# Kernel optimization log

Hardware: AMD Instinct MI355X
Metric: run time of the kernel (lower is better)

Reference implementation:

```python
import jax, jax.numpy as jnp
import numpy as np

DEPTH, LENGTH, WIDTH, NUM_CLASSES = 8, 32, 32, 8
STD_POSITION = 1.0
STD_INTENSITY = 3.0


def setup_inputs() -> dict:
    key = jax.random.key(0)
    k1, k2 = jax.random.split(key)
    patch = jax.random.normal(k1, (DEPTH, LENGTH, WIDTH), dtype=jnp.float32)
    prob = jax.random.uniform(k2, (DEPTH, LENGTH, WIDTH, NUM_CLASSES), dtype=jnp.float32)
    return {"patch": patch, "prob": prob, "k": NUM_CLASSES}


def _dist_weight():
    # Matches torch.meshgrid(arange(depth), arange(length), arange(width)) with 'ij' indexing,
    # then row-major flatten. dist_weight[i,j] = exp(-||pos_i - pos_j||^2 / std_position^2)
    gx, gy, gz = jnp.meshgrid(
        jnp.arange(DEPTH, dtype=jnp.float32),
        jnp.arange(LENGTH, dtype=jnp.float32),
        jnp.arange(WIDTH, dtype=jnp.float32),
        indexing="ij",
    )
    x, y, z = gx.ravel(), gy.ravel(), gz.ravel()  # each [n]
    sq = (
        jnp.square(x[:, None] - x[None, :])
        + jnp.square(y[:, None] - y[None, :])
        + jnp.square(z[:, None] - z[None, :])
    )  # [n, n]
    return jnp.exp(-sq / (STD_POSITION ** 2))


def reference(patch, prob, k):
    n = DEPTH * LENGTH * WIDTH
    f = patch.reshape(-1)  # [n]
    # intensity_weight is .detach()ed in the original -> stop_gradient for faithfulness
    intensity = jax.lax.stop_gradient(
        jnp.exp(-jnp.square((f[:, None] - f[None, :]) / STD_INTENSITY))
    )  # [n, n]
    W = intensity * _dist_weight()  # [n, n]

    P = prob.reshape(n, k)  # row-major flatten matches torch.reshape of prob[:,:,:,t]
    WP = W @ P  # [n, k]
    num = jnp.sum(P * WP, axis=0)            # per-class p^T W p
    den = P.T @ (W @ jnp.ones((n,), W.dtype))  # per-class p^T W 1
    loss = jnp.float32(k) - jnp.sum(num / den)
    return loss.astype(jnp.float32)
```

## Files before the change

kernel.cpp:

```cpp
#include <hip/hip_runtime.h>

#define N       8192
#define NCLS    8
#define ROWS_PB 4
#define GRID    (N / ROWS_PB)

__global__ __launch_bounds__(256) void sncut_rows(const float* __restrict__ f,
                                                  const float* __restrict__ P,
                                                  float* __restrict__ partials)
{
    const int tid  = threadIdx.x;
    const int lane = tid & 63;
    const int wave = tid >> 6;
    const int i    = blockIdx.x * ROWS_PB + wave;

    const int zi = i & 31, yi = (i >> 5) & 31, xi = i >> 10;
    const float fi = f[i];

    float v0 = 0.f, v1 = 0.f, v2 = 0.f, v3 = 0.f;
    float v4 = 0.f, v5 = 0.f, v6 = 0.f, v7 = 0.f;
    float vr = 0.f;

    if (lane < 63) {
        const int oy = lane / 9, oz = lane - oy * 9;

        int y0 = yi - 3; y0 = y0 < 0 ? 0 : (y0 > 25 ? 25 : y0);
        int z0 = zi - 4; z0 = z0 < 0 ? 0 : (z0 > 23 ? 23 : z0);
        int x0 = xi - 3; x0 = x0 < 0 ? 0 : (x0 > 1 ? 1 : x0);

        const int yj = y0 + oy, zj = z0 + oz;
        const int dy = yi - yj, dz = zi - zj;
        const float base = (float)(dy * dy + dz * dz);
        const int jcol = (yj << 5) + zj;

        #pragma unroll
        for (int k = 0; k < 7; ++k) {
            const int xj = x0 + k;
            const int dx = xi - xj;
            const int j  = (xj << 10) + jcol;
            const float df  = fi - f[j];
            const float arg = df * df * (1.0f / 9.0f) + (base + (float)(dx * dx));
            const float w   = __expf(-arg);
            const float4 p0 = *reinterpret_cast<const float4*>(P + (size_t)j * NCLS);
            const float4 p1 = *reinterpret_cast<const float4*>(P + (size_t)j * NCLS + 4);
            v0 += w * p0.x; v1 += w * p0.y; v2 += w * p0.z; v3 += w * p0.w;
            v4 += w * p1.x; v5 += w * p1.y; v6 += w * p1.z; v7 += w * p1.w;
            vr += w;
        }
    }

    float vals[9] = {v0, v1, v2, v3, v4, v5, v6, v7, vr};
    #pragma unroll
    for (int v = 0; v < 9; ++v) {
        float x = vals[v];
        #pragma unroll
        for (int off = 32; off > 0; off >>= 1)
            x += __shfl_down(x, off, 64);
        vals[v] = x;
    }

    __shared__ float sh[ROWS_PB][16];
    if (lane == 0) {
        const float4 p0 = *reinterpret_cast<const float4*>(P + (size_t)i * NCLS);
        const float4 p1 = *reinterpret_cast<const float4*>(P + (size_t)i * NCLS + 4);
        sh[wave][0]  = p0.x * vals[0];
        sh[wave][1]  = p0.y * vals[1];
        sh[wave][2]  = p0.z * vals[2];
        sh[wave][3]  = p0.w * vals[3];
        sh[wave][4]  = p1.x * vals[4];
        sh[wave][5]  = p1.y * vals[5];
        sh[wave][6]  = p1.z * vals[6];
        sh[wave][7]  = p1.w * vals[7];
        sh[wave][8]  = p0.x * vals[8];
        sh[wave][9]  = p0.y * vals[8];
        sh[wave][10] = p0.z * vals[8];
        sh[wave][11] = p0.w * vals[8];
        sh[wave][12] = p1.x * vals[8];
        sh[wave][13] = p1.y * vals[8];
        sh[wave][14] = p1.z * vals[8];
        sh[wave][15] = p1.w * vals[8];
    }
    __syncthreads();
    if (tid < 16) {
        const float s = sh[0][tid] + sh[1][tid] + sh[2][tid] + sh[3][tid];
        partials[(size_t)blockIdx.x * 16 + tid] = s;
    }
}

__global__ __launch_bounds__(1024) void sncut_final(const float* __restrict__ partials,
                                                    float* __restrict__ out)
{
    const int tid = threadIdx.x;
    const int e = tid & 15;
    const int g = tid >> 4;

    float s = 0.f;
    #pragma unroll
    for (int m = 0; m < GRID / 64; ++m)
        s += partials[(size_t)(g + m * 64) * 16 + e];

    __shared__ float acc[64][17];
    acc[g][e] = s;
    __syncthreads();

    __shared__ float sums[16];
    if (tid < 16) {
        float t = 0.f;
        #pragma unroll
        for (int g2 = 0; g2 < 64; ++g2) t += acc[g2][tid];
        sums[tid] = t;
    }
    __syncthreads();
    if (tid == 0) {
        float loss = (float)NCLS;
        #pragma unroll
        for (int t = 0; t < NCLS; ++t) loss -= sums[t] / sums[NCLS + t];
        out[0] = loss;
    }
}

extern "C" void kernel_launch(void* const* d_in, const int* in_sizes, int n_in,
                              void* d_out, int out_size, void* d_ws, size_t ws_size,
                              hipStream_t stream) {
    const float* f = (const float*)d_in[0];
    const float* P = (const float*)d_in[1];

    float* partials = (float*)d_ws;

    sncut_rows<<<GRID, 256, 0, stream>>>(f, P, partials);
    sncut_final<<<1, 1024, 0, stream>>>(partials, (float*)d_out);
}
```

Measured before the change: 67.60 us.

## Stage shared neighborhood tile in LDS for eight rows per block

Each block now handles eight consecutive z-rows and first cooperatively loads the union of their 7x7x16 neighborhood (f and P split into float2 planes) into shared memory. The per-row window loop then reads from LDS instead of issuing scattered global loads. This removes redundant global/L2 traffic across neighboring rows but adds a barrier, a staging phase, and larger blocks with more LDS use per block.

```diff
diff --git a/kernel.cpp b/kernel.cpp
--- a/kernel.cpp
+++ b/kernel.cpp
@@ -2,19 +2,49 @@
 
 #define N       8192
 #define NCLS    8
-#define ROWS_PB 4
+#define ROWS_PB 8
 #define GRID    (N / ROWS_PB)
+#define NCELL   784
 
-__global__ __launch_bounds__(256) void sncut_rows(const float* __restrict__ f,
+__global__ __launch_bounds__(512) void sncut_rows(const float* __restrict__ f,
                                                   const float* __restrict__ P,
                                                   float* __restrict__ partials)
 {
+    __shared__ float2 Pl[4][NCELL];
+    __shared__ float  fl[NCELL];
+    __shared__ float  sh[ROWS_PB][16];
+
     const int tid  = threadIdx.x;
     const int lane = tid & 63;
     const int wave = tid >> 6;
-    const int i    = blockIdx.x * ROWS_PB + wave;
+    const int i0   = blockIdx.x * ROWS_PB;
 
-    const int zi = i & 31, yi = (i >> 5) & 31, xi = i >> 10;
+    const int zi0 = i0 & 31;
+    const int yi  = (i0 >> 5) & 31;
+    const int xi  = i0 >> 10;
+
+    int Y0 = yi - 3;  Y0 = Y0 < 0 ? 0 : (Y0 > 25 ? 25 : Y0);
+    int X0 = xi - 3;  X0 = X0 < 0 ? 0 : (X0 > 1 ? 1 : X0);
+    int Z0 = zi0 - 4; Z0 = Z0 < 0 ? 0 : (Z0 > 16 ? 16 : Z0);
+
+    for (int c = tid; c < NCELL; c += 512) {
+        const int xc = c / 112;
+        const int r  = c - xc * 112;
+        const int yc = r >> 4;
+        const int zc = r & 15;
+        const int j  = ((X0 + xc) << 10) + ((Y0 + yc) << 5) + (Z0 + zc);
+        const float4 p0 = *reinterpret_cast<const float4*>(P + (size_t)j * NCLS);
+        const float4 p1 = *reinterpret_cast<const float4*>(P + (size_t)j * NCLS + 4);
+        Pl[0][c] = make_float2(p0.x, p0.y);
+        Pl[1][c] = make_float2(p0.z, p0.w);
+        Pl[2][c] = make_float2(p1.x, p1.y);
+        Pl[3][c] = make_float2(p1.z, p1.w);
+        fl[c]    = f[j];
+    }
+    __syncthreads();
+
+    const int   i  = i0 + wave;
+    const int   zi = zi0 + wave;
     const float fi = f[i];
 
     float v0 = 0.f, v1 = 0.f, v2 = 0.f, v3 = 0.f;
@@ -24,27 +54,26 @@
     if (lane < 63) {
         const int oy = lane / 9, oz = lane - oy * 9;
 
-        int y0 = yi - 3; y0 = y0 < 0 ? 0 : (y0 > 25 ? 25 : y0);
         int z0 = zi - 4; z0 = z0 < 0 ? 0 : (z0 > 23 ? 23 : z0);
-        int x0 = xi - 3; x0 = x0 < 0 ? 0 : (x0 > 1 ? 1 : x0);
 
-        const int yj = y0 + oy, zj = z0 + oz;
-        const int dy = yi - yj, dz = zi - zj;
+        const int dy = yi - (Y0 + oy);
+        const int dz = zi - (z0 + oz);
         const float base = (float)(dy * dy + dz * dz);
-        const int jcol = (yj << 5) + zj;
+        const int cb = oy * 16 + (z0 - Z0) + oz;
 
         #pragma unroll
         for (int k = 0; k < 7; ++k) {
-            const int xj = x0 + k;
-            const int dx = xi - xj;
-            const int j  = (xj << 10) + jcol;
-            const float df  = fi - f[j];
+            const int dx = xi - (X0 + k);
+            const int c  = cb + k * 112;
+            const float df  = fi - fl[c];
             const float arg = df * df * (1.0f / 9.0f) + (base + (float)(dx * dx));
             const float w   = __expf(-arg);
-            const float4 p0 = *reinterpret_cast<const float4*>(P + (size_t)j * NCLS);
-            const float4 p1 = *reinterpret_cast<const float4*>(P + (size_t)j * NCLS + 4);
-            v0 += w * p0.x; v1 += w * p0.y; v2 += w * p0.z; v3 += w * p0.w;
-            v4 += w * p1.x; v5 += w * p1.y; v6 += w * p1.z; v7 += w * p1.w;
+            const float2 a  = Pl[0][c];
+            const float2 b  = Pl[1][c];
+            const float2 cc = Pl[2][c];
+            const float2 d  = Pl[3][c];
+            v0 += w * a.x;  v1 += w * a.y;  v2 += w * b.x;  v3 += w * b.y;
+            v4 += w * cc.x; v5 += w * cc.y; v6 += w * d.x;  v7 += w * d.y;
             vr += w;
         }
     }
@@ -59,7 +88,6 @@
         vals[v] = x;
     }
 
-    __shared__ float sh[ROWS_PB][16];
     if (lane == 0) {
         const float4 p0 = *reinterpret_cast<const float4*>(P + (size_t)i * NCLS);
         const float4 p1 = *reinterpret_cast<const float4*>(P + (size_t)i * NCLS + 4);
@@ -82,7 +110,9 @@
     }
     __syncthreads();
     if (tid < 16) {
-        const float s = sh[0][tid] + sh[1][tid] + sh[2][tid] + sh[3][tid];
+        float s = 0.f;
+        #pragma unroll
+        for (int wv = 0; wv < ROWS_PB; ++wv) s += sh[wv][tid];
         partials[(size_t)blockIdx.x * 16 + tid] = s;
     }
 }
@@ -127,6 +157,6 @@
 
     float* partials = (float*)d_ws;
 
-    sncut_rows<<<GRID, 256, 0, stream>>>(f, P, partials);
+    sncut_rows<<<GRID, 512, 0, stream>>>(f, P, partials);
     sncut_final<<<1, 1024, 0, stream>>>(partials, (float*)d_out);
 }
```

Result: slower. 69.25 us (+2.4%).

## Fuse final reduction into row kernel via last-block atomic ticket

Applied to the files above, without the earlier changes.

Merges the two launches into one kernel. Each block writes its partials, then takes an atomic ticket, and the last block to arrive reduces all partials and writes the loss. This removes the second launch and its gap. In exchange it adds a threadfence and an atomic per block, and makes the final reduction run with 256 threads instead of 1024. The ticket relies on a monotonically increasing counter in uninitialized workspace, with a base offset read from workspace and a modulo on GRID, which is fragile.

```diff
diff --git a/kernel.cpp b/kernel.cpp
--- a/kernel.cpp
+++ b/kernel.cpp
@@ -4,10 +4,14 @@
 #define NCLS    8
 #define ROWS_PB 4
 #define GRID    (N / ROWS_PB)
+#define PART_DW (GRID * 16)
+#define TICKET_DW 33280
+#define BASE_DW   34304
 
-__global__ __launch_bounds__(256) void sncut_rows(const float* __restrict__ f,
-                                                  const float* __restrict__ P,
-                                                  float* __restrict__ partials)
+__global__ __launch_bounds__(256) void sncut_fused(const float* __restrict__ f,
+                                                   const float* __restrict__ P,
+                                                   float* __restrict__ ws,
+                                                   float* __restrict__ out)
 {
     const int tid  = threadIdx.x;
     const int lane = tid & 63;
@@ -83,31 +87,39 @@
     __syncthreads();
     if (tid < 16) {
         const float s = sh[0][tid] + sh[1][tid] + sh[2][tid] + sh[3][tid];
-        partials[(size_t)blockIdx.x * 16 + tid] = s;
+        ws[(size_t)blockIdx.x * 16 + tid] = s;
     }
-}
 
-__global__ __launch_bounds__(1024) void sncut_final(const float* __restrict__ partials,
-                                                    float* __restrict__ out)
-{
-    const int tid = threadIdx.x;
+    __shared__ int isLast;
+    __syncthreads();
+    if (tid == 0) {
+        __threadfence();
+        unsigned int* ticket = (unsigned int*)ws + TICKET_DW;
+        const unsigned int base = *((volatile unsigned int*)ws + BASE_DW);
+        const unsigned int old  = atomicAdd(ticket, 1u);
+        isLast = (((old - base) & (unsigned int)(GRID - 1)) == (unsigned int)(GRID - 1));
+    }
+    __syncthreads();
+    if (!isLast) return;
+
+    __threadfence();
+
     const int e = tid & 15;
     const int g = tid >> 4;
+    float s2 = 0.f;
+    #pragma unroll 16
+    for (int m = 0; m < GRID / 16; ++m)
+        s2 += ws[(size_t)(g + m * 16) * 16 + e];
 
-    float s = 0.f;
-    #pragma unroll
-    for (int m = 0; m < GRID / 64; ++m)
-        s += partials[(size_t)(g + m * 64) * 16 + e];
-
-    __shared__ float acc[64][17];
-    acc[g][e] = s;
+    __shared__ float acc[16][17];
+    acc[g][e] = s2;
     __syncthreads();
 
     __shared__ float sums[16];
     if (tid < 16) {
         float t = 0.f;
         #pragma unroll
-        for (int g2 = 0; g2 < 64; ++g2) t += acc[g2][tid];
+        for (int g2 = 0; g2 < 16; ++g2) t += acc[g2][tid];
         sums[tid] = t;
     }
     __syncthreads();
@@ -125,8 +137,5 @@
     const float* f = (const float*)d_in[0];
     const float* P = (const float*)d_in[1];
 
-    float* partials = (float*)d_ws;
-
-    sncut_rows<<<GRID, 256, 0, stream>>>(f, P, partials);
-    sncut_final<<<1, 1024, 0, stream>>>(partials, (float*)d_out);
+    sncut_fused<<<GRID, 256, 0, stream>>>(f, P, (float*)d_ws, (float*)d_out);
 }
```

New measurement: 100.9 us. 1.49x slower.
